# Kernel tuning notes

Measured on AMD Instinct MI355X. Metric: run time of the kernel, lower is better.

The kernel has to match this reference:

```python
import jax, jax.numpy as jnp
import numpy as np

HEADS = 8

def setup_inputs() -> dict:
    key = jax.random.key(0)
    ks = jax.random.split(key, 10)
    B, S, E = 2, 2048, 512
    q = jax.random.normal(ks[0], (B, S, E), jnp.float32)
    k = jax.random.normal(ks[1], (B, S, E), jnp.float32)
    v = jax.random.normal(ks[2], (B, S, E), jnp.float32)
    mask = jnp.zeros((S, S), jnp.float32)  # additive mask [s_q, s_k]
    scale = 0.02
    Wq = jax.random.normal(ks[3], (E, E), jnp.float32) * scale
    bq = jax.random.normal(ks[4], (E,), jnp.float32) * scale
    Wk = jax.random.normal(ks[5], (E, E), jnp.float32) * scale
    bk = jax.random.normal(ks[6], (E,), jnp.float32) * scale
    Wv = jax.random.normal(ks[7], (E, E), jnp.float32) * scale
    bv = jax.random.normal(ks[8], (E,), jnp.float32) * scale
    return {"q": q, "k": k, "v": v, "mask": mask,
            "Wq": Wq, "bq": bq, "Wk": Wk, "bk": bk, "Wv": Wv, "bv": bv}

def reference(q, k, v, mask, Wq, bq, Wk, bk, Wv, bv):
    H = HEADS
    b, s_q, _ = q.shape
    s_k = k.shape[1]
    s_v = v.shape[1]
    # NOTE: faithful to source: row-major view(b, H, s, -1) WITHOUT transposing
    # seq/head axes first (quirk of the original module).
    K = jnp.swapaxes((k @ Wk.T + bk).reshape(b, H, s_k, -1), 2, 3)  # [b,H,dh,s_k]
    Q = (q @ Wq.T + bq).reshape(b, H, s_q, -1)                      # [b,H,s_q,dh]
    V = (v @ Wv.T + bv).reshape(b, H, s_v, -1)                      # [b,H,s_v,dh]
    # NOTE: original scales by sqrt(K.shape[-1]) AFTER the transpose, i.e. sqrt(s_k)
    scores = (Q @ K) / jnp.sqrt(jnp.asarray(s_k, jnp.float32))      # [b,H,s_q,s_k]
    scores = scores + mask[:s_q, :s_k]
    attn = jax.nn.softmax(scores, axis=-1)
    out = (attn @ V).reshape(b, s_q, -1)  # [b, s_q, e]
    return out
```

## Files before the change

kernel.cpp:

```cpp
#include <hip/hip_runtime.h>


#define SEQ 2048
#define EMB 512
#define DH  64
#define MROWS 4096
#define NROWS 32768

typedef float  v4f __attribute__((ext_vector_type(4)));
typedef short  v8s __attribute__((ext_vector_type(8)));
typedef __fp16 v2h __attribute__((ext_vector_type(2)));

static __device__ __forceinline__ unsigned int f2bf(float f) {
    unsigned int u = __float_as_uint(f);
    u += 0x7fffu + ((u >> 16) & 1u);
    return u >> 16;
}
static __device__ __forceinline__ unsigned int pack2(float a, float b) {
    return f2bf(a) | (f2bf(b) << 16);
}
static __device__ __forceinline__ unsigned int packh2(float a, float b) {
    v2h h = __builtin_amdgcn_cvt_pkrtz(a, b);
    return __builtin_bit_cast(unsigned int, h);
}

__global__ __launch_bounds__(256, 3) void proj_kernel(
    const float* __restrict__ q, const float* __restrict__ k, const float* __restrict__ v,
    const float* __restrict__ Wq, const float* __restrict__ bq,
    const float* __restrict__ Wk, const float* __restrict__ bk,
    const float* __restrict__ Wv, const float* __restrict__ bv,
    const float* __restrict__ mask,
    unsigned short* __restrict__ Qbf, unsigned short* __restrict__ Kbf,
    unsigned short* __restrict__ Vbf, float* __restrict__ maskT,
    unsigned int* __restrict__ flags)
{
    __shared__ __align__(16) char smem[27648];
    const int tid = threadIdx.x;

    if (blockIdx.x >= 768) {
        const int mb2 = blockIdx.x - 768;
        const int rb = mb2 >> 5, kt = mb2 & 31;
        float* tile = maskT + ((size_t)rb * 32 + kt) * 8192;
        float4 vals[8];
        bool any = false;
#pragma unroll
        for (int i = 0; i < 8; ++i) {
            int s = tid + i * 256;
            int l  = s & 63;
            int cb = (s >> 6) & 3;
            int g  = (s >> 8) & 1;
            int w2 = (s >> 9) & 3;
            int qd2 = l >> 4, n2 = l & 15;
            vals[i] = *(const float4*)&mask[
                (size_t)(rb * 128 + w2 * 32 + g * 16 + n2) * SEQ + kt * 64 + cb * 16 + qd2 * 4];
            any = any | (vals[i].x != 0.f) | (vals[i].y != 0.f)
                      | (vals[i].z != 0.f) | (vals[i].w != 0.f);
        }
        unsigned int* nzp = (unsigned int*)smem;
        if (tid == 0) *nzp = 0u;
        __syncthreads();
        if (any) *nzp = 1u;
        __syncthreads();
        if (*nzp) {
#pragma unroll
            for (int i = 0; i < 8; ++i) {
                int s = tid + i * 256;
                *(float4*)&tile[(size_t)s * 4] = vals[i];
            }
            if (tid == 0) atomicOr(&flags[rb], 1u << kt);
        }
        return;
    }

    char* As = smem;
    char* Ws = smem + 9216;

    const int id  = blockIdx.x;
    const int pos = id & 31;
    const int nb  = pos >> 3;
    const int unit = (id >> 5) * 8 + (pos & 7);
    const int mb = unit & 63;
    const int z  = unit >> 6;

    const float* A    = (z == 0) ? q  : (z == 1) ? k  : v;
    const float* W    = (z == 0) ? Wq : (z == 1) ? Wk : Wv;
    const float* bias = (z == 0) ? bq : (z == 1) ? bk : bv;
    unsigned short* Cg = (z == 0) ? Qbf : (z == 1) ? Kbf : Vbf;

    const int w    = tid >> 6;
    const int lane = tid & 63;
    const int qd   = lane >> 4;
    const int n    = lane & 15;
    const int m0 = mb * 64, n0 = nb * 128;

    float4 areg[4], wreg[8];
#pragma unroll
    for (int i = 0; i < 4; ++i) {
        int c = tid + i * 256;
        areg[i] = *(const float4*)&A[(size_t)(m0 + (c >> 4)) * EMB + (c & 15) * 4];
    }
#pragma unroll
    for (int i = 0; i < 8; ++i) {
        int c = tid + i * 256;
        wreg[i] = *(const float4*)&W[(size_t)(n0 + (c >> 4)) * EMB + (c & 15) * 4];
    }

    v4f acc[8];
#pragma unroll
    for (int cb = 0; cb < 8; ++cb) acc[cb] = (v4f)0.f;

#pragma unroll 1
    for (int kt = 0; kt < 8; ++kt) {
        __syncthreads();
#pragma unroll
        for (int i = 0; i < 4; ++i) {
            int c = tid + i * 256;
            uint2 pk = { pack2(areg[i].x, areg[i].y), pack2(areg[i].z, areg[i].w) };
            *(uint2*)&As[(c >> 4) * 144 + (c & 15) * 8] = pk;
        }
#pragma unroll
        for (int i = 0; i < 8; ++i) {
            int c = tid + i * 256;
            uint2 pk = { pack2(wreg[i].x, wreg[i].y), pack2(wreg[i].z, wreg[i].w) };
            *(uint2*)&Ws[(c >> 4) * 144 + (c & 15) * 8] = pk;
        }
        __syncthreads();

        if (kt + 1 < 8) {
#pragma unroll
            for (int i = 0; i < 4; ++i) {
                int c = tid + i * 256;
                areg[i] = *(const float4*)&A[(size_t)(m0 + (c >> 4)) * EMB + (kt+1) * 64 + (c & 15) * 4];
            }
#pragma unroll
            for (int i = 0; i < 8; ++i) {
                int c = tid + i * 256;
                wreg[i] = *(const float4*)&W[(size_t)(n0 + (c >> 4)) * EMB + (kt+1) * 64 + (c & 15) * 4];
            }
        }

#pragma unroll
        for (int ks = 0; ks < 2; ++ks) {
            v8s af = *(const v8s*)&As[(w * 16 + n) * 144 + ks * 64 + qd * 16];
#pragma unroll
            for (int cb = 0; cb < 8; ++cb) {
                v8s bfr = *(const v8s*)&Ws[(cb * 16 + n) * 144 + ks * 64 + qd * 16];
                acc[cb] = __builtin_amdgcn_mfma_f32_16x16x32_bf16(af, bfr, acc[cb], 0, 0, 0);
            }
        }
    }

    const float osc = (z == 0) ? 0.02209708691207961f : 1.0f;
    float bb[8];
#pragma unroll
    for (int cb = 0; cb < 8; ++cb) bb[cb] = bias[n0 + cb * 16 + n];
#pragma unroll
    for (int cb = 0; cb < 8; ++cb)
#pragma unroll
        for (int r = 0; r < 4; ++r) acc[cb][r] = (acc[cb][r] + bb[cb]) * osc;

    __syncthreads();
    short* Ct = (short*)smem;
#pragma unroll
    for (int cb = 0; cb < 8; ++cb)
#pragma unroll
        for (int r = 0; r < 4; ++r)
            Ct[(w * 16 + qd * 4 + r) * 136 + cb * 16 + n] = (short)f2bf(acc[cb][r]);
    __syncthreads();
    const int rr = tid >> 2, q4 = tid & 3;
#pragma unroll
    for (int i = 0; i < 4; ++i) {
        uint4 t4 = *(const uint4*)&smem[rr * 272 + q4 * 64 + i * 16];
        *(uint4*)&Cg[(size_t)(m0 + rr) * EMB + n0 + q4 * 32 + i * 8] = t4;
    }
}

__global__ __launch_bounds__(256) void vtrans_kernel(
    const unsigned short* __restrict__ Vbf, unsigned short* __restrict__ VtT)
{
    __shared__ unsigned short T[64 * 136];
    const int bh = blockIdx.x, kt = blockIdx.y;
    const int tid = threadIdx.x;
    const unsigned short* Vh = Vbf + (size_t)bh * (SEQ * DH) + (size_t)kt * 64 * DH;
#pragma unroll
    for (int i = 0; i < 2; ++i) {
        int c = tid + i * 256;
        int s_l = c >> 3, ch = c & 7;
        uint4 t4 = *(const uint4*)&Vh[c * 8];
        const unsigned short* e = (const unsigned short*)&t4;
#pragma unroll
        for (int j = 0; j < 8; ++j)
            T[(ch * 8 + j) * 136 + s_l] = e[j];
    }
    __syncthreads();
    unsigned short* Ot = VtT + ((size_t)bh * 32 + kt) * (64 * 64);
    const int d = tid >> 2, sq = tid & 3;
#pragma unroll
    for (int i = 0; i < 2; ++i) {
        uint4 t4 = *(const uint4*)&T[d * 136 + sq * 16 + i * 8];
        *(uint4*)&Ot[d * 64 + sq * 16 + i * 8] = t4;
    }
}

template <int SPLITS>
__global__ __launch_bounds__(256, 4) void attn_kernel(
    const unsigned short* __restrict__ Qbf, const unsigned short* __restrict__ Kbf,
    const unsigned short* __restrict__ VtT,
    const float* __restrict__ maskT, const float* __restrict__ maskf,
    const unsigned int* __restrict__ flags,
    unsigned short* __restrict__ Opart, float* __restrict__ ml,
    float* __restrict__ out)
{
    __shared__ __align__(16) char smem[36864];
    char* Ks  = smem;
    char* Vts = smem + 9216;

    const int tid  = threadIdx.x;
    const int w    = tid >> 6;
    const int lane = tid & 63;
    const int qd   = lane >> 4;
    const int n    = lane & 15;
    char* Ps = smem + 18432 + w * 4608;

    const int id = blockIdx.x;
    const int rb = ((id >> 3) & 1) * 8 + (id & 7);
    const int bh = (id >> 4) & 15;
    const int kq = id >> 8;
    const int KT0 = kq * (32 / SPLITS), KT1 = KT0 + 32 / SPLITS;

    const unsigned short* Qh = Qbf + (size_t)bh * (SEQ * DH);
    const unsigned short* Kh = Kbf + (size_t)bh * (SEQ * DH);
    const unsigned short* Vth = VtT + (size_t)bh * 32 * 4096;

    const unsigned int fl = (SPLITS > 1) ? flags[rb] : 0u;

    v8s qf[2][2];
#pragma unroll
    for (int g = 0; g < 2; ++g) {
        const size_t qrow = (size_t)(rb * 128 + w * 32 + g * 16 + n);
#pragma unroll
        for (int ks = 0; ks < 2; ++ks)
            qf[g][ks] = *(const v8s*)&Qh[qrow * DH + ks * 32 + qd * 8];
    }

    uint4 kreg[2], vreg[2];
#pragma unroll
    for (int p = 0; p < 2; ++p) {
        int c = tid + p * 256;
        kreg[p] = *(const uint4*)&Kh[(size_t)KT0 * 4096 + c * 8];
        vreg[p] = *(const uint4*)&Vth[(size_t)KT0 * 4096 + c * 8];
    }

    float l_[2] = { 0.f, 0.f };
    v4f oacc[2][4];
#pragma unroll
    for (int g = 0; g < 2; ++g)
#pragma unroll
        for (int cb = 0; cb < 4; ++cb) oacc[g][cb] = (v4f)0.f;

#pragma unroll 1
    for (int kt = KT0; kt < KT1; ++kt) {
        __syncthreads();
#pragma unroll
        for (int p = 0; p < 2; ++p) {
            int c = tid + p * 256;
            *(uint4*)&Ks [(c >> 3) * 144 + (c & 7) * 16] = kreg[p];
            *(uint4*)&Vts[(c >> 3) * 144 + (c & 7) * 16] = vreg[p];
        }
        __syncthreads();

        v4f sacc[2][4];
        float4 mk[2][4];
        if (SPLITS > 1) {
            if (fl & (1u << kt)) {
                const float* tileF = maskT + ((size_t)rb * 32 + kt) * 8192;
#pragma unroll
                for (int g = 0; g < 2; ++g)
#pragma unroll
                    for (int cb = 0; cb < 4; ++cb)
                        sacc[g][cb] = *(const v4f*)&tileF[
                            (size_t)((((w * 2 + g) * 4 + cb) * 64) + qd * 16 + n) * 4];
            } else {
#pragma unroll
                for (int g = 0; g < 2; ++g)
#pragma unroll
                    for (int cb = 0; cb < 4; ++cb) sacc[g][cb] = (v4f)0.f;
            }
        } else {
#pragma unroll
            for (int g = 0; g < 2; ++g) {
                const size_t mrow = (size_t)(rb * 128 + w * 32 + g * 16 + n);
#pragma unroll
                for (int cb = 0; cb < 4; ++cb) {
                    mk[g][cb] = *(const float4*)&maskf[mrow * SEQ + kt * 64 + cb * 16 + qd * 4];
                    sacc[g][cb] = (v4f)0.f;
                }
            }
        }

        if (kt + 1 < KT1) {
#pragma unroll
            for (int p = 0; p < 2; ++p) {
                int c = tid + p * 256;
                kreg[p] = *(const uint4*)&Kh[(size_t)(kt + 1) * 4096 + c * 8];
                vreg[p] = *(const uint4*)&Vth[(size_t)(kt + 1) * 4096 + c * 8];
            }
        }

#pragma unroll
        for (int ks = 0; ks < 2; ++ks)
#pragma unroll
            for (int cb = 0; cb < 4; ++cb) {
                v8s kf = *(const v8s*)&Ks[(cb * 16 + n) * 144 + ks * 64 + qd * 16];
#pragma unroll
                for (int g = 0; g < 2; ++g)
                    sacc[g][cb] = __builtin_amdgcn_mfma_f32_16x16x32_bf16(kf, qf[g][ks], sacc[g][cb], 0, 0, 0);
            }

#pragma unroll
        for (int g = 0; g < 2; ++g) {
            float rs = 0.f;
            float pv[4][4];
#pragma unroll
            for (int cb = 0; cb < 4; ++cb) {
                if (SPLITS == 1) {
                    sacc[g][cb][0] += mk[g][cb].x; sacc[g][cb][1] += mk[g][cb].y;
                    sacc[g][cb][2] += mk[g][cb].z; sacc[g][cb][3] += mk[g][cb].w;
                }
#pragma unroll
                for (int r = 0; r < 4; ++r) {
                    float e = __expf(sacc[g][cb][r]);
                    pv[cb][r] = e;
                    rs += e;
                }
            }
            rs += __shfl_xor(rs, 16);
            rs += __shfl_xor(rs, 32);
            l_[g] += rs;
#pragma unroll
            for (int cb = 0; cb < 4; ++cb) {
                uint2 pk = { pack2(pv[cb][0], pv[cb][1]), pack2(pv[cb][2], pv[cb][3]) };
                *(uint2*)&Ps[(g * 16 + n) * 144 + cb * 32 + qd * 8] = pk;
            }
        }

#pragma unroll
        for (int ks = 0; ks < 2; ++ks) {
            v8s pf[2];
#pragma unroll
            for (int g = 0; g < 2; ++g)
                pf[g] = *(const v8s*)&Ps[(g * 16 + n) * 144 + ks * 64 + qd * 16];
#pragma unroll
            for (int cb = 0; cb < 4; ++cb) {
                v8s vf = *(const v8s*)&Vts[(cb * 16 + n) * 144 + ks * 64 + qd * 16];
#pragma unroll
                for (int g = 0; g < 2; ++g)
                    oacc[g][cb] = __builtin_amdgcn_mfma_f32_16x16x32_bf16(vf, pf[g], oacc[g][cb], 0, 0, 0);
            }
        }
    }

    if (SPLITS == 1) {
#pragma unroll
        for (int g = 0; g < 2; ++g) {
            const float inv = 1.0f / l_[g];
#pragma unroll
            for (int cb = 0; cb < 4; ++cb)
#pragma unroll
                for (int r = 0; r < 4; ++r) oacc[g][cb][r] *= inv;
        }
    } else {
        if (qd == 0) {
#pragma unroll
            for (int g = 0; g < 2; ++g) {
                const size_t row = (size_t)bh * SEQ + rb * 128 + w * 32 + g * 16 + n;
                ml[(size_t)kq * NROWS + row] = l_[g];
            }
        }
    }
    __syncthreads();
#pragma unroll
    for (int g = 0; g < 2; ++g)
#pragma unroll
        for (int cb = 0; cb < 4; ++cb)
            *(v4f*)&smem[(w * 32 + g * 16 + n) * 272 + cb * 64 + qd * 16] = oacc[g][cb];
    __syncthreads();
    const int r_l = tid >> 1, hf = tid & 1;
    if (SPLITS == 1) {
        float* dst = &out[((size_t)bh * SEQ + rb * 128 + r_l) * DH + hf * 32];
#pragma unroll
        for (int i = 0; i < 8; ++i) {
            float4 t4 = *(const float4*)&smem[r_l * 272 + hf * 128 + i * 16];
            *(float4*)&dst[i * 4] = t4;
        }
    } else {
        unsigned short* dst = &Opart[((size_t)kq * NROWS + (size_t)bh * SEQ + rb * 128 + r_l) * DH + hf * 32];
#pragma unroll
        for (int i = 0; i < 4; ++i) {
            float4 f0 = *(const float4*)&smem[r_l * 272 + hf * 128 + i * 32];
            float4 f1 = *(const float4*)&smem[r_l * 272 + hf * 128 + i * 32 + 16];
            uint4 o = { packh2(f0.x, f0.y), packh2(f0.z, f0.w),
                        packh2(f1.x, f1.y), packh2(f1.z, f1.w) };
            *(uint4*)&dst[i * 8] = o;
        }
    }
}

__global__ __launch_bounds__(256) void combine_kernel(
    const unsigned int* __restrict__ Opart, const float* __restrict__ ml,
    float* __restrict__ out, int splits)
{
    const int tid = threadIdx.x;
    const size_t row = (size_t)blockIdx.x * 16 + (tid >> 4);
    const int d4 = (tid & 15) * 4;
    float denom = 0.f;
    float4 o = make_float4(0.f, 0.f, 0.f, 0.f);
    for (int s = 0; s < splits; ++s) {
        denom += ml[(size_t)s * NROWS + row];
        uint2 u = *(const uint2*)&Opart[((size_t)s * NROWS + row) * 32 + (d4 >> 1)];
        v2h h0 = __builtin_bit_cast(v2h, u.x);
        v2h h1 = __builtin_bit_cast(v2h, u.y);
        o.x += (float)h0.x; o.y += (float)h0.y;
        o.z += (float)h1.x; o.w += (float)h1.y;
    }
    const float inv = 1.0f / denom;
    o.x *= inv; o.y *= inv; o.z *= inv; o.w *= inv;
    *(float4*)&out[row * DH + d4] = o;
}

extern "C" void kernel_launch(void* const* d_in, const int* in_sizes, int n_in,
                              void* d_out, int out_size, void* d_ws, size_t ws_size,
                              hipStream_t stream) {
    const float* q    = (const float*)d_in[0];
    const float* k    = (const float*)d_in[1];
    const float* v    = (const float*)d_in[2];
    const float* mask = (const float*)d_in[3];
    const float* Wq   = (const float*)d_in[4];
    const float* bq   = (const float*)d_in[5];
    const float* Wk   = (const float*)d_in[6];
    const float* bk   = (const float*)d_in[7];
    const float* Wv   = (const float*)d_in[8];
    const float* bv   = (const float*)d_in[9];

    char* ws = (char*)d_ws;
    const size_t MB = 1024 * 1024;
    unsigned short* Qbf   = (unsigned short*)(ws + 0);
    unsigned short* Kbf   = (unsigned short*)(ws + 4 * MB);
    unsigned short* VtT   = (unsigned short*)(ws + 8 * MB);
    unsigned short* Opart = (unsigned short*)(ws + 12 * MB);
    unsigned short* Vbf   = (unsigned short*)(ws + 12 * MB);
    float*          mlp   = (float*)(ws + 28 * MB);
    unsigned int*   flags = (unsigned int*)(ws + 28 * MB + 512 * 1024);
    float*          maskT = (float*)(ws + 29 * MB);

    const size_t need_split = 45 * MB;
    const bool do_split = ws_size >= need_split;

    if (do_split) {
        (void)hipMemsetAsync(flags, 0, 64, stream);
        proj_kernel<<<1280, 256, 0, stream>>>(q, k, v, Wq, bq, Wk, bk, Wv, bv,
                                              mask, Qbf, Kbf, Vbf, maskT, flags);
        dim3 tgrid(16, 32);
        vtrans_kernel<<<tgrid, 256, 0, stream>>>(Vbf, VtT);
        attn_kernel<4><<<1024, 256, 0, stream>>>(Qbf, Kbf, VtT, maskT, mask, flags,
                                                 Opart, mlp, (float*)d_out);
        combine_kernel<<<NROWS / 16, 256, 0, stream>>>((const unsigned int*)Opart,
                                                       mlp, (float*)d_out, 4);
    } else {
        proj_kernel<<<768, 256, 0, stream>>>(q, k, v, Wq, bq, Wk, bk, Wv, bv,
                                             mask, Qbf, Kbf, Vbf, maskT, flags);
        dim3 tgrid(16, 32);
        vtrans_kernel<<<tgrid, 256, 0, stream>>>(Vbf, VtT);
        attn_kernel<1><<<256, 256, 0, stream>>>(Qbf, Kbf, VtT, maskT, mask, flags,
                                                Opart, mlp, (float*)d_out);
    }
}
```

Before: 174.7 us.

## Read K/V fragments directly from global memory, drop LDS staging and barriers

Removes the shared-memory staging of K and V tiles, along with the two block barriers per iteration, and has each lane load its MFMA operand fragments straight from global memory (relying on L1/L2 reuse across waves). It also remaps block IDs so that neighbouring blocks share the same row block across heads, and adds s_setprio around the MFMA sections. The intent is to eliminate LDS write traffic and synchronisation stalls. In exchange, global load latency is exposed without explicit prefetching, and redundant loads across the four waves now go to cache.

```diff
diff --git a/kernel.cpp b/kernel.cpp
--- a/kernel.cpp
+++ b/kernel.cpp
@@ -211,21 +211,19 @@
     unsigned short* __restrict__ Opart, float* __restrict__ ml,
     float* __restrict__ out)
 {
-    __shared__ __align__(16) char smem[36864];
-    char* Ks  = smem;
-    char* Vts = smem + 9216;
-
+    __shared__ __align__(16) char smem[34816];
     const int tid  = threadIdx.x;
     const int w    = tid >> 6;
     const int lane = tid & 63;
     const int qd   = lane >> 4;
     const int n    = lane & 15;
-    char* Ps = smem + 18432 + w * 4608;
+    char* Ps = smem + w * 4608;
 
     const int id = blockIdx.x;
-    const int rb = ((id >> 3) & 1) * 8 + (id & 7);
-    const int bh = (id >> 4) & 15;
-    const int kq = id >> 8;
+    const int bh = (id & 7) * 2 + ((id >> 3) & 1);
+    const int unit = id >> 4;
+    const int rb = unit & 15;
+    const int kq = unit >> 4;
     const int KT0 = kq * (32 / SPLITS), KT1 = KT0 + 32 / SPLITS;
 
     const unsigned short* Qh = Qbf + (size_t)bh * (SEQ * DH);
@@ -243,13 +241,7 @@
             qf[g][ks] = *(const v8s*)&Qh[qrow * DH + ks * 32 + qd * 8];
     }
 
-    uint4 kreg[2], vreg[2];
-#pragma unroll
-    for (int p = 0; p < 2; ++p) {
-        int c = tid + p * 256;
-        kreg[p] = *(const uint4*)&Kh[(size_t)KT0 * 4096 + c * 8];
-        vreg[p] = *(const uint4*)&Vth[(size_t)KT0 * 4096 + c * 8];
-    }
+    const int fro = n * 64 + qd * 8;
 
     float l_[2] = { 0.f, 0.f };
     v4f oacc[2][4];
@@ -260,14 +252,8 @@
 
 #pragma unroll 1
     for (int kt = KT0; kt < KT1; ++kt) {
-        __syncthreads();
-#pragma unroll
-        for (int p = 0; p < 2; ++p) {
-            int c = tid + p * 256;
-            *(uint4*)&Ks [(c >> 3) * 144 + (c & 7) * 16] = kreg[p];
-            *(uint4*)&Vts[(c >> 3) * 144 + (c & 7) * 16] = vreg[p];
-        }
-        __syncthreads();
+        const unsigned short* Kt = Kh  + (size_t)kt * 4096;
+        const unsigned short* Vt = Vth + (size_t)kt * 4096;
 
         v4f sacc[2][4];
         float4 mk[2][4];
@@ -298,24 +284,17 @@
             }
         }
 
-        if (kt + 1 < KT1) {
-#pragma unroll
-            for (int p = 0; p < 2; ++p) {
-                int c = tid + p * 256;
-                kreg[p] = *(const uint4*)&Kh[(size_t)(kt + 1) * 4096 + c * 8];
-                vreg[p] = *(const uint4*)&Vth[(size_t)(kt + 1) * 4096 + c * 8];
-            }
-        }
-
+        __builtin_amdgcn_s_setprio(1);
 #pragma unroll
         for (int ks = 0; ks < 2; ++ks)
 #pragma unroll
             for (int cb = 0; cb < 4; ++cb) {
-                v8s kf = *(const v8s*)&Ks[(cb * 16 + n) * 144 + ks * 64 + qd * 16];
+                v8s kf = *(const v8s*)&Kt[cb * 1024 + ks * 32 + fro];
 #pragma unroll
                 for (int g = 0; g < 2; ++g)
                     sacc[g][cb] = __builtin_amdgcn_mfma_f32_16x16x32_bf16(kf, qf[g][ks], sacc[g][cb], 0, 0, 0);
             }
+        __builtin_amdgcn_s_setprio(0);
 
 #pragma unroll
         for (int g = 0; g < 2; ++g) {
@@ -344,6 +323,7 @@
             }
         }
 
+        __builtin_amdgcn_s_setprio(1);
 #pragma unroll
         for (int ks = 0; ks < 2; ++ks) {
             v8s pf[2];
@@ -352,12 +332,13 @@
                 pf[g] = *(const v8s*)&Ps[(g * 16 + n) * 144 + ks * 64 + qd * 16];
 #pragma unroll
             for (int cb = 0; cb < 4; ++cb) {
-                v8s vf = *(const v8s*)&Vts[(cb * 16 + n) * 144 + ks * 64 + qd * 16];
+                v8s vf = *(const v8s*)&Vt[cb * 1024 + ks * 32 + fro];
 #pragma unroll
                 for (int g = 0; g < 2; ++g)
                     oacc[g][cb] = __builtin_amdgcn_mfma_f32_16x16x32_bf16(vf, pf[g], oacc[g][cb], 0, 0, 0);
             }
         }
+        __builtin_amdgcn_s_setprio(0);
     }
 
     if (SPLITS == 1) {
```

New measurement: 186.9 us. +7.0%, slower.
